# Kernel optimization log

Measured on AMD Instinct MI355X. Metric: run time of the kernel, lower is better.

The kernel has to match this reference:

```python
import jax, jax.numpy as jnp
import numpy as np


def setup_inputs() -> dict:
    key = jax.random.key(0)
    k1, k2, k3, k4 = jax.random.split(key, 4)
    B, L, T = 8, 2048, 1024
    Dh, Dg, Dp = 1024, 768, 256
    H = jax.random.normal(k1, (B, L, Dh), dtype=jnp.float32)
    G = jax.random.normal(k2, (B, T, Dg), dtype=jnp.float32)
    # nn.Linear(d_g, d_proj, bias=False).weight -> [d_proj, d_g]
    Wq = jax.random.normal(k3, (Dp, Dg), dtype=jnp.float32) * (Dg ** -0.5)
    Wk = jax.random.normal(k4, (Dp, Dh), dtype=jnp.float32) * (Dh ** -0.5)
    return {"H": H, "G": G, "Wq": Wq, "Wk": Wk}


def reference(H, G, Wq, Wk):
    # GO-token queries attend over protein residues; values are the raw H.
    # The torch module computes this with streaming chunks + online LSE,
    # which is mathematically identical to a single stable softmax attention.
    d_proj = Wq.shape[0]
    scale = d_proj ** -0.5
    Q = jnp.einsum('btg,pg->btp', G, Wq)          # [B,T,Dp]
    K = jnp.einsum('blh,ph->blp', H, Wk)          # [B,L,Dp]
    logits = jnp.einsum('btp,blp->btl', Q, K) * scale  # [B,T,L] fp32
    alpha = jax.nn.softmax(logits, axis=-1)
    # denominator clamp matches torch's s.clamp_min(1e-20) (no-op for unmasked)
    Z = jnp.einsum('btl,blh->bth', alpha, H)      # [B,T,Dh]
    return Z
```

## Files before the change

kernel.cpp:

```cpp
#include <hip/hip_runtime.h>
#include <hip/hip_bf16.h>
#include <type_traits>


typedef float    f32x4  __attribute__((ext_vector_type(4)));
typedef __bf16   bf16x8 __attribute__((ext_vector_type(8)));
typedef unsigned short u16x8 __attribute__((ext_vector_type(8)));

__device__ __forceinline__ unsigned short f2bf(float f) {
    union { __bf16 b; unsigned short u; } c;
    c.b = (__bf16)f;
    return c.u;
}
__device__ __forceinline__ float bf2f(unsigned short u) {
    union { unsigned u; float f; } x; x.u = ((unsigned)u) << 16;
    return x.f;
}
__device__ __forceinline__ void gload_lds16(const unsigned short* g, unsigned short* l) {
    __builtin_amdgcn_global_load_lds(
        (const __attribute__((address_space(1))) void*)g,
        (__attribute__((address_space(3))) void*)l, 16, 0, 0);
}

__global__ __launch_bounds__(256) void kn_castw(const float* __restrict__ Wq,
                                                const float* __restrict__ Wk,
                                                unsigned short* __restrict__ Wqbf,
                                                unsigned short* __restrict__ Wkbf,
                                                float* __restrict__ rowsum,
                                                int nq8, int nk8, int nrs4) {
    int tid = threadIdx.x;
    if (blockIdx.x == 0) {
        f32x4 z = {};
        for (int j = tid; j < nrs4; j += 256)
            *(f32x4*)(rowsum + (size_t)j * 4) = z;
    }
    int i = blockIdx.x * 256 + tid;
    const float* src;
    unsigned short* dst;
    int idx;
    if (i < nq8) { idx = i; src = Wq; dst = Wqbf; }
    else { idx = i - nq8; if (idx >= nk8) return; src = Wk; dst = Wkbf; }
    f32x4 a = *(const f32x4*)(src + (size_t)idx * 8);
    f32x4 b = *(const f32x4*)(src + (size_t)idx * 8 + 4);
    u16x8 o;
#pragma unroll
    for (int j = 0; j < 4; ++j) { o[j] = f2bf(a[j]); o[4 + j] = f2bf(b[j]); }
    *(u16x8*)(dst + (size_t)idx * 8) = o;
}

__global__ __launch_bounds__(256) void kn_transp(const float* __restrict__ H,
                                                 unsigned short* __restrict__ HT,
                                                 unsigned short* __restrict__ Hbf,
                                                 int L, int D) {
    __shared__ float tile[64][65];
    int b = blockIdx.z;
    const float* src = H + (size_t)b * L * D;
    unsigned short* dstT = HT + (size_t)b * L * D;
    unsigned short* dstN = Hbf + (size_t)b * L * D;
    int l0 = blockIdx.y * 64, d0 = blockIdx.x * 64;
    int rh = threadIdx.x >> 3;
    int c8 = (threadIdx.x & 7) * 8;

#pragma unroll
    for (int i = 0; i < 2; ++i) {
        int r = rh + i * 32;
        const float* p = &src[(size_t)(l0 + r) * D + d0 + c8];
        f32x4 v0 = *(const f32x4*)p;
        f32x4 v1 = *(const f32x4*)(p + 4);
        u16x8 o;
#pragma unroll
        for (int j = 0; j < 4; ++j) {
            o[j] = f2bf(v0[j]); o[4 + j] = f2bf(v1[j]);
            tile[r][c8 + j] = v0[j];
            tile[r][c8 + 4 + j] = v1[j];
        }
        *(u16x8*)&dstN[(size_t)(l0 + r) * D + d0 + c8] = o;
    }
    __syncthreads();
#pragma unroll
    for (int i = 0; i < 2; ++i) {
        int d = rh + i * 32;
        u16x8 o;
#pragma unroll
        for (int j = 0; j < 8; ++j) o[j] = f2bf(tile[c8 + j][d]);
        *(u16x8*)&dstT[(size_t)(d0 + d) * L + l0 + c8] = o;
    }
}

__device__ __forceinline__ void qproj_body(char* smem_raw,
                                           const float* __restrict__ A,
                                           const unsigned short* __restrict__ B,
                                           unsigned short* __restrict__ C,
                                           int N, int K, int t) {
    unsigned short* sA = (unsigned short*)smem_raw;
    unsigned short* sB = sA + 32 * 64;
    float* st = (float*)smem_raw;

    int tid = threadIdx.x;
    int by = t >> 1;
    int bx = t & 1;
    const float* Ab = A + (size_t)by * 32 * K;
    const unsigned short* Bb = B + (size_t)bx * 128 * K;

    int lane = tid & 63;
    int wid = tid >> 6;
    int lr = lane & 15;
    int lg = lane >> 4;
    int xoff = (lane & 7) << 3;

    f32x4 acc[2][2] = {};

    for (int k0 = 0; k0 < K; k0 += 64) {
#pragma unroll
        for (int c = 0; c < 4; ++c) {
            int ch = c * 256 + tid;
            int row = ch >> 3;
            int g8 = (ch & 7) ^ (row & 7);
            gload_lds16(Bb + (size_t)row * K + k0 + g8 * 8, sB + ch * 8);
        }
        {
            int ch = tid;
            int row = ch >> 3;
            const float* srcp = Ab + (size_t)row * K + k0 + (ch & 7) * 8;
            f32x4 v0 = *(const f32x4*)srcp;
            f32x4 v1 = *(const f32x4*)(srcp + 4);
            u16x8 o;
#pragma unroll
            for (int j = 0; j < 4; ++j) { o[j] = f2bf(v0[j]); o[4 + j] = f2bf(v1[j]); }
            int sl = (ch & 7) ^ (row & 7);
            *(u16x8*)&sA[row * 64 + sl * 8] = o;
        }
        __syncthreads();
#pragma unroll
        for (int kk = 0; kk < 2; ++kk) {
            int kb = (kk * 32 + lg * 8) ^ xoff;
            bf16x8 af[2], bfr[2];
#pragma unroll
            for (int m = 0; m < 2; ++m)
                af[m] = *(const bf16x8*)&sA[(m * 16 + lr) * 64 + kb];
#pragma unroll
            for (int n = 0; n < 2; ++n)
                bfr[n] = *(const bf16x8*)&sB[(wid * 32 + n * 16 + lr) * 64 + kb];
#pragma unroll
            for (int m = 0; m < 2; ++m)
#pragma unroll
                for (int n = 0; n < 2; ++n)
                    acc[m][n] = __builtin_amdgcn_mfma_f32_16x16x32_bf16(af[m], bfr[n], acc[m][n], 0, 0, 0);
        }
        __syncthreads();
    }

#pragma unroll
    for (int m = 0; m < 2; ++m) {
        int r0 = m * 16 + lg * 4;
#pragma unroll
        for (int n = 0; n < 2; ++n) {
            int c0 = wid * 32 + n * 16 + lr;
#pragma unroll
            for (int j = 0; j < 4; ++j)
                st[(r0 + j) * 132 + c0] = acc[m][n][j];
        }
    }
    __syncthreads();
    int r  = tid >> 3;
    int c0 = (tid & 7) * 16;
    size_t grow = (size_t)(by * 32 + r) * N + bx * 128 + c0;
#pragma unroll
    for (int g = 0; g < 2; ++g) {
        f32x4 a = *(const f32x4*)&st[r * 132 + c0 + g * 8];
        f32x4 b = *(const f32x4*)&st[r * 132 + c0 + g * 8 + 4];
        u16x8 o;
#pragma unroll
        for (int j = 0; j < 4; ++j) { o[j] = f2bf(a[j]); o[4 + j] = f2bf(b[j]); }
        *(u16x8*)&C[grow + g * 8] = o;
    }
}

__device__ __forceinline__ void kproj_body(char* smem_raw,
                                           const unsigned short* __restrict__ A,
                                           const unsigned short* __restrict__ B,
                                           unsigned short* __restrict__ C,
                                           int N, int K, int t) {
    unsigned short* sA = (unsigned short*)smem_raw;
    unsigned short* sB = sA + 64 * 64;
    float* st = (float*)smem_raw;

    int tid = threadIdx.x;
    int by = t >> 1;
    int bx = t & 1;
    const unsigned short* Ab = A + (size_t)by * 64 * K;
    const unsigned short* Bb = B + (size_t)bx * 128 * K;

    int lane = tid & 63;
    int wid = tid >> 6;
    int wr = wid >> 1, wc = wid & 1;
    int lr = lane & 15;
    int lg = lane >> 4;
    int xoff = (lane & 7) << 3;

    f32x4 acc[2][4] = {};

    for (int k0 = 0; k0 < K; k0 += 64) {
#pragma unroll
        for (int c = 0; c < 2; ++c) {
            int ch = c * 256 + tid;
            int row = ch >> 3;
            int g8 = (ch & 7) ^ (row & 7);
            gload_lds16(Ab + (size_t)row * K + k0 + g8 * 8, sA + ch * 8);
        }
#pragma unroll
        for (int c = 0; c < 4; ++c) {
            int ch = c * 256 + tid;
            int row = ch >> 3;
            int g8 = (ch & 7) ^ (row & 7);
            gload_lds16(Bb + (size_t)row * K + k0 + g8 * 8, sB + ch * 8);
        }
        __syncthreads();
#pragma unroll
        for (int kk = 0; kk < 2; ++kk) {
            int kb = (kk * 32 + lg * 8) ^ xoff;
            bf16x8 af[2], bfr[4];
#pragma unroll
            for (int m = 0; m < 2; ++m)
                af[m] = *(const bf16x8*)&sA[(wr * 32 + m * 16 + lr) * 64 + kb];
#pragma unroll
            for (int n = 0; n < 4; ++n)
                bfr[n] = *(const bf16x8*)&sB[(wc * 64 + n * 16 + lr) * 64 + kb];
#pragma unroll
            for (int m = 0; m < 2; ++m)
#pragma unroll
                for (int n = 0; n < 4; ++n)
                    acc[m][n] = __builtin_amdgcn_mfma_f32_16x16x32_bf16(af[m], bfr[n], acc[m][n], 0, 0, 0);
        }
        __syncthreads();
    }

#pragma unroll
    for (int m = 0; m < 2; ++m) {
        int r0 = wr * 32 + m * 16 + lg * 4;
#pragma unroll
        for (int n = 0; n < 4; ++n) {
            int c0 = wc * 64 + n * 16 + lr;
#pragma unroll
            for (int j = 0; j < 4; ++j)
                st[(r0 + j) * 132 + c0] = acc[m][n][j];
        }
    }
    __syncthreads();
    int r  = tid >> 2;
    int c0 = (tid & 3) * 32;
    size_t grow = (size_t)(by * 64 + r) * N + bx * 128 + c0;
#pragma unroll
    for (int g = 0; g < 4; ++g) {
        f32x4 a = *(const f32x4*)&st[r * 132 + c0 + g * 8];
        f32x4 b = *(const f32x4*)&st[r * 132 + c0 + g * 8 + 4];
        u16x8 o;
#pragma unroll
        for (int j = 0; j < 4; ++j) { o[j] = f2bf(a[j]); o[4 + j] = f2bf(b[j]); }
        *(u16x8*)&C[grow + g * 8] = o;
    }
}

__global__ __launch_bounds__(256) void kn_proj(const unsigned short* __restrict__ Hbf,
                                               const unsigned short* __restrict__ Wkbf,
                                               unsigned short* __restrict__ Kbf,
                                               const float* __restrict__ G,
                                               const unsigned short* __restrict__ Wqbf,
                                               unsigned short* __restrict__ Qbf,
                                               int Dp, int Dh, int Dg) {
    __shared__ __align__(16) char smem_raw[64 * 132 * 4];
    int wg = blockIdx.x;
    if (wg < 512) kproj_body(smem_raw, Hbf, Wkbf, Kbf, Dp, Dh, wg);
    else          qproj_body(smem_raw, G, Wqbf, Qbf, Dp, Dg, wg - 512);
}

__global__ __launch_bounds__(512) void kn_sgemm(const unsigned short* __restrict__ A,
                                                const unsigned short* __restrict__ B,
                                                unsigned short* __restrict__ C,
                                                float* __restrict__ rowsum,
                                                int N, int K, int Trows,
                                                long batchA, long batchB, long batchC,
                                                float scale, int gxs) {
    __shared__ __align__(16) char smem_raw[49152];
    unsigned short* base = (unsigned short*)smem_raw;
    float* st = (float*)smem_raw;

    int tid = threadIdx.x;
    int wg = blockIdx.x;
    int bz = wg & 7;
    int t = wg >> 3;
    int by = t >> gxs;
    int bx = t & ((1 << gxs) - 1);

    const unsigned short* Ab = A + (size_t)bz * batchA + (size_t)by * 256 * K;
    const unsigned short* Bb = B + (size_t)bz * batchB + (size_t)bx * 128 * K;
    unsigned short* Cb = C + (size_t)bz * batchC;
    float* rs = rowsum + (size_t)bz * Trows;

    int lane = tid & 63;
    int wid = tid >> 6;
    int wr = wid >> 1, wc = wid & 1;
    int lr = lane & 15;
    int lg = lane >> 4;
    int xoff = (lane & 7) << 3;

    f32x4 acc[4][4] = {};

    for (int k0 = 0; k0 < K; k0 += 64) {
#pragma unroll
        for (int c = 0; c < 6; ++c) {
            int ch = c * 512 + tid;
            if (ch < 2048) {
                int row = ch >> 3;
                int g8 = (ch & 7) ^ (row & 7);
                gload_lds16(Ab + (size_t)row * K + k0 + g8 * 8, base + ch * 8);
            } else {
                int bc = ch - 2048;
                int row = bc >> 3;
                int g8 = (bc & 7) ^ (row & 7);
                gload_lds16(Bb + (size_t)row * K + k0 + g8 * 8, base + 16384 + bc * 8);
            }
        }
        __syncthreads();
#pragma unroll
        for (int kk = 0; kk < 2; ++kk) {
            int kb = (kk * 32 + lg * 8) ^ xoff;
            bf16x8 af[4], bfr[4];
#pragma unroll
            for (int m = 0; m < 4; ++m)
                af[m] = *(const bf16x8*)&base[(wr * 64 + m * 16 + lr) * 64 + kb];
#pragma unroll
            for (int n = 0; n < 4; ++n)
                bfr[n] = *(const bf16x8*)&base[16384 + (wc * 64 + n * 16 + lr) * 64 + kb];
#pragma unroll
            for (int m = 0; m < 4; ++m)
#pragma unroll
                for (int n = 0; n < 4; ++n)
                    acc[m][n] = __builtin_amdgcn_mfma_f32_16x16x32_bf16(af[m], bfr[n], acc[m][n], 0, 0, 0);
        }
        __syncthreads();
    }

#pragma unroll
    for (int q = 0; q < 4; ++q) {
        if (wr == q) {
#pragma unroll
            for (int m = 0; m < 4; ++m) {
                int rl = m * 16 + lg * 4;
#pragma unroll
                for (int n = 0; n < 4; ++n) {
                    int col = wc * 64 + n * 16 + lr;
#pragma unroll
                    for (int j = 0; j < 4; ++j)
                        st[(rl + j) * 132 + col] = acc[m][n][j] * scale;
                }
            }
        }
        __syncthreads();
        int r = tid >> 3;
        int c0 = (tid & 7) * 16;
        int grow_r = by * 256 + q * 64 + r;
        size_t grow = (size_t)grow_r * N + bx * 128 + c0;
        float psum = 0.f;
#pragma unroll
        for (int g = 0; g < 2; ++g) {
            f32x4 a = *(const f32x4*)&st[r * 132 + c0 + g * 8];
            f32x4 b = *(const f32x4*)&st[r * 132 + c0 + g * 8 + 4];
            u16x8 o;
#pragma unroll
            for (int j = 0; j < 4; ++j) {
                o[j]     = f2bf(__expf(a[j]));
                o[4 + j] = f2bf(__expf(b[j]));
                psum += bf2f(o[j]) + bf2f(o[4 + j]);
            }
            *(u16x8*)&Cb[grow + g * 8] = o;
        }
        psum += __shfl_xor(psum, 1);
        psum += __shfl_xor(psum, 2);
        psum += __shfl_xor(psum, 4);
        if ((tid & 7) == 0)
            atomicAdd(&rs[grow_r], psum);
        __syncthreads();
    }
}

__global__ __launch_bounds__(512) void kn_pv(const unsigned short* __restrict__ A,
                                             const unsigned short* __restrict__ B,
                                             float* __restrict__ C,
                                             const float* __restrict__ rowsum,
                                             int N, int K, int Trows,
                                             long batchA, long batchB, long batchC,
                                             int gxs) {
    __shared__ __align__(16) char smem_raw[3 * 49152];
    unsigned short* base = (unsigned short*)smem_raw;
    float* st = (float*)smem_raw;

    int tid = threadIdx.x;
    int wg = blockIdx.x;
    int bz = wg & 7;
    int t = wg >> 3;
    int by = t >> gxs;
    int bx = t & ((1 << gxs) - 1);

    const unsigned short* Ab = A + (size_t)bz * batchA + (size_t)by * 256 * K;
    const unsigned short* Bb = B + (size_t)bz * batchB + (size_t)bx * 128 * K;
    float* Cb = C + (size_t)bz * batchC;
    const float* rs = rowsum + (size_t)bz * Trows;

    int lane = tid & 63;
    int wid = tid >> 6;
    int wr = wid >> 1, wc = wid & 1;
    int lr = lane & 15;
    int lg = lane >> 4;
    int xoff = (lane & 7) << 3;

    f32x4 acc[4][4] = {};
    bf16x8 fA0[4], fB0[4], fA1[4], fB1[4];

    auto STAGE_HALF = [&](int buf, int k0, int half) {
        unsigned short* dA = base + buf * 24576;
        unsigned short* dB = dA + 16384;
#pragma unroll
        for (int c = 0; c < 3; ++c) {
            int ch = half * 1536 + c * 512 + tid;
            if (ch < 2048) {
                int row = ch >> 3;
                int g8 = (ch & 7) ^ (row & 7);
                gload_lds16(Ab + (size_t)row * K + k0 + g8 * 8, dA + ch * 8);
            } else {
                int bc = ch - 2048;
                int row = bc >> 3;
                int g8 = (bc & 7) ^ (row & 7);
                gload_lds16(Bb + (size_t)row * K + k0 + g8 * 8, dB + bc * 8);
            }
        }
    };
    auto LDFRAG = [&](int buf, int kk, bf16x8* fa, bf16x8* fb) {
        unsigned short* pA = base + buf * 24576;
        unsigned short* pB = pA + 16384;
        int kb = (kk * 32 + lg * 8) ^ xoff;
#pragma unroll
        for (int m = 0; m < 4; ++m)
            fa[m] = *(const bf16x8*)&pA[(wr * 64 + m * 16 + lr) * 64 + kb];
#pragma unroll
        for (int n = 0; n < 4; ++n)
            fb[n] = *(const bf16x8*)&pB[(wc * 64 + n * 16 + lr) * 64 + kb];
    };

    int nt = K / 64;
    STAGE_HALF(0, 0, 0);   STAGE_HALF(0, 0, 1);
    STAGE_HALF(1, 64, 0);  STAGE_HALF(1, 64, 1);
    asm volatile("s_waitcnt vmcnt(6)" ::: "memory");
    __builtin_amdgcn_s_barrier();
    LDFRAG(0, 0, fA0, fB0);

    int cur = 0;
    for (int tt = 0; tt < nt; ++tt) {
        int nb  = (cur >= 1) ? cur - 1 : 2;
        int nxt = (cur == 2) ? 0 : cur + 1;
        if (tt + 2 < nt) STAGE_HALF(nb, (tt + 2) * 64, 0);
        LDFRAG(cur, 1, fA1, fB1);
        __builtin_amdgcn_sched_barrier(0);
        __builtin_amdgcn_s_setprio(1);
#pragma unroll
        for (int m = 0; m < 4; ++m)
#pragma unroll
            for (int n = 0; n < 4; ++n)
                acc[m][n] = __builtin_amdgcn_mfma_f32_16x16x32_bf16(fA0[m], fB0[n], acc[m][n], 0, 0, 0);
        __builtin_amdgcn_s_setprio(0);
        __builtin_amdgcn_sched_barrier(0);
        if (tt + 2 < nt) STAGE_HALF(nb, (tt + 2) * 64, 1);
        __builtin_amdgcn_sched_barrier(0);
        __builtin_amdgcn_s_setprio(1);
#pragma unroll
        for (int m = 0; m < 4; ++m)
#pragma unroll
            for (int n = 0; n < 4; ++n)
                acc[m][n] = __builtin_amdgcn_mfma_f32_16x16x32_bf16(fA1[m], fB1[n], acc[m][n], 0, 0, 0);
        __builtin_amdgcn_s_setprio(0);
        __builtin_amdgcn_sched_barrier(0);
        if (tt + 1 < nt) {
            if (tt + 2 < nt) asm volatile("s_waitcnt vmcnt(6)" ::: "memory");
            else             asm volatile("s_waitcnt vmcnt(0)" ::: "memory");
            LDFRAG(nxt, 0, fA0, fB0);
            __builtin_amdgcn_sched_barrier(0);
            __builtin_amdgcn_s_barrier();
        }
        cur = nxt;
    }
    __syncthreads();

#pragma unroll
    for (int q = 0; q < 4; ++q) {
        if (wr == q) {
#pragma unroll
            for (int m = 0; m < 4; ++m) {
                int rl = m * 16 + lg * 4;
#pragma unroll
                for (int n = 0; n < 4; ++n) {
                    int col = wc * 64 + n * 16 + lr;
#pragma unroll
                    for (int j = 0; j < 4; ++j)
                        st[(rl + j) * 132 + col] = acc[m][n][j];
                }
            }
        }
        __syncthreads();
        int r = tid >> 3;
        int c0 = (tid & 7) * 16;
        float inv = 1.0f / rs[by * 256 + q * 64 + r];
        size_t grow = (size_t)(by * 256 + q * 64 + r) * N + bx * 128 + c0;
#pragma unroll
        for (int g = 0; g < 4; ++g) {
            f32x4 v = *(const f32x4*)&st[r * 132 + c0 + g * 4];
#pragma unroll
            for (int j = 0; j < 4; ++j) v[j] *= inv;
            *(f32x4*)&Cb[grow + g * 4] = v;
        }
        __syncthreads();
    }
}

extern "C" void kernel_launch(void* const* d_in, const int* in_sizes, int n_in,
                              void* d_out, int out_size, void* d_ws, size_t ws_size,
                              hipStream_t stream) {
    constexpr int B = 8, L = 2048, T = 1024, Dh = 1024, Dg = 768, Dp = 256;
    const float* H  = (const float*)d_in[0];
    const float* G  = (const float*)d_in[1];
    const float* Wq = (const float*)d_in[2];
    const float* Wk = (const float*)d_in[3];
    float* Z = (float*)d_out;

    unsigned short* Qbf  = (unsigned short*)d_ws;
    unsigned short* Kbf  = Qbf + (size_t)B * T * Dp;
    unsigned short* HT   = Kbf + (size_t)B * L * Dp;
    unsigned short* S    = HT  + (size_t)B * Dh * L;
    unsigned short* Hbf  = S   + (size_t)B * T * L;
    unsigned short* Wqbf = Hbf + (size_t)B * L * Dh;
    unsigned short* Wkbf = Wqbf + (size_t)Dp * Dg;
    float* rowsum = (float*)(Wkbf + (size_t)Dp * Dh);

    int nq8 = Dp * Dg / 8, nk8 = Dp * Dh / 8;
    kn_castw<<<(nq8 + nk8 + 255) / 256, 256, 0, stream>>>
        (Wq, Wk, Wqbf, Wkbf, rowsum, nq8, nk8, B * T / 4);

    kn_transp<<<dim3(Dh / 64, L / 64, B), dim3(256), 0, stream>>>(H, HT, Hbf, L, Dh);

    kn_proj<<<1024, 256, 0, stream>>>(Hbf, Wkbf, Kbf, G, Wqbf, Qbf, Dp, Dh, Dg);

    kn_sgemm<<<(T / 256) * (L / 128) * B, 512, 0, stream>>>
        (Qbf, Kbf, S, rowsum, L, Dp, T, (long)T * Dp, (long)L * Dp, (long)T * L, 0.0625f, 4);

    kn_pv<<<(T / 256) * (Dh / 128) * B, 512, 0, stream>>>
        (S, HT, Z, rowsum, Dh, L, T, (long)T * L, (long)Dh * L, (long)T * Dh, 3);
}
```

Measured before the change: 124.2 us.

## Fold weight cast into transpose kernel and simplify PV GEMM to double buffering

Removes the separate weight-cast/rowsum-zero kernel launch by folding that work into the H transpose kernel, using flattened block ids. Replaces the PV GEMM's hand-scheduled triple-buffered pipeline (half-stage loads, register-prefetched fragments, setprio and sched barriers) with a plain double-buffered loop that issues the next stage and syncs once per iteration. This saves a launch and cuts LDS from 144KB to 96KB, which may allow more occupancy. The cost is weaker load/compute overlap and more full barriers in the main GEMM.

After: 119.3 us (median of 2 runs). -3.9%, faster.

```diff
diff --git a/kernel.cpp b/kernel.cpp
--- a/kernel.cpp
+++ b/kernel.cpp
@@ -22,36 +22,15 @@
         (__attribute__((address_space(3))) void*)l, 16, 0, 0);
 }
 
-__global__ __launch_bounds__(256) void kn_castw(const float* __restrict__ Wq,
-                                                const float* __restrict__ Wk,
-                                                unsigned short* __restrict__ Wqbf,
-                                                unsigned short* __restrict__ Wkbf,
-                                                float* __restrict__ rowsum,
-                                                int nq8, int nk8, int nrs4) {
-    int tid = threadIdx.x;
-    if (blockIdx.x == 0) {
-        f32x4 z = {};
-        for (int j = tid; j < nrs4; j += 256)
-            *(f32x4*)(rowsum + (size_t)j * 4) = z;
-    }
-    int i = blockIdx.x * 256 + tid;
-    const float* src;
-    unsigned short* dst;
-    int idx;
-    if (i < nq8) { idx = i; src = Wq; dst = Wqbf; }
-    else { idx = i - nq8; if (idx >= nk8) return; src = Wk; dst = Wkbf; }
-    f32x4 a = *(const f32x4*)(src + (size_t)idx * 8);
-    f32x4 b = *(const f32x4*)(src + (size_t)idx * 8 + 4);
-    u16x8 o;
-#pragma unroll
-    for (int j = 0; j < 4; ++j) { o[j] = f2bf(a[j]); o[4 + j] = f2bf(b[j]); }
-    *(u16x8*)(dst + (size_t)idx * 8) = o;
-}
-
 __global__ __launch_bounds__(256) void kn_transp(const float* __restrict__ H,
                                                  unsigned short* __restrict__ HT,
                                                  unsigned short* __restrict__ Hbf,
-                                                 int L, int D) {
+                                                 const float* __restrict__ Wq,
+                                                 const float* __restrict__ Wk,
+                                                 unsigned short* __restrict__ Wqbf,
+                                                 unsigned short* __restrict__ Wkbf,
+                                                 float* __restrict__ rowsum,
+                                                 int L, int D, int nq8, int nk8, int nrs4) {
     __shared__ float tile[64][65];
     int b = blockIdx.z;
     const float* src = H + (size_t)b * L * D;
@@ -60,6 +39,29 @@
     int l0 = blockIdx.y * 64, d0 = blockIdx.x * 64;
     int rh = threadIdx.x >> 3;
     int c8 = (threadIdx.x & 7) * 8;
+
+    int fid = blockIdx.x + gridDim.x * (blockIdx.y + gridDim.y * blockIdx.z);
+    if (fid == 0) {
+        f32x4 z = {};
+        for (int j = threadIdx.x; j < nrs4; j += 256)
+            *(f32x4*)(rowsum + (size_t)j * 4) = z;
+    }
+    {
+        int i = fid * 256 + threadIdx.x;
+        if (i < nq8 + nk8) {
+            const float* s;
+            unsigned short* dp;
+            int idx;
+            if (i < nq8) { idx = i; s = Wq; dp = Wqbf; }
+            else         { idx = i - nq8; s = Wk; dp = Wkbf; }
+            f32x4 a = *(const f32x4*)(s + (size_t)idx * 8);
+            f32x4 bb = *(const f32x4*)(s + (size_t)idx * 8 + 4);
+            u16x8 o;
+#pragma unroll
+            for (int j = 0; j < 4; ++j) { o[j] = f2bf(a[j]); o[4 + j] = f2bf(bb[j]); }
+            *(u16x8*)(dp + (size_t)idx * 8) = o;
+        }
+    }
 
 #pragma unroll
     for (int i = 0; i < 2; ++i) {
@@ -391,7 +393,7 @@
                                              int N, int K, int Trows,
                                              long batchA, long batchB, long batchC,
                                              int gxs) {
-    __shared__ __align__(16) char smem_raw[3 * 49152];
+    __shared__ __align__(16) char smem_raw[2 * 49152];
     unsigned short* base = (unsigned short*)smem_raw;
     float* st = (float*)smem_raw;
 
@@ -415,14 +417,13 @@
     int xoff = (lane & 7) << 3;
 
     f32x4 acc[4][4] = {};
-    bf16x8 fA0[4], fB0[4], fA1[4], fB1[4];
-
-    auto STAGE_HALF = [&](int buf, int k0, int half) {
+
+    auto STAGE = [&](int buf, int k0) {
         unsigned short* dA = base + buf * 24576;
         unsigned short* dB = dA + 16384;
 #pragma unroll
-        for (int c = 0; c < 3; ++c) {
-            int ch = half * 1536 + c * 512 + tid;
+        for (int c = 0; c < 6; ++c) {
+            int ch = c * 512 + tid;
             if (ch < 2048) {
                 int row = ch >> 3;
                 int g8 = (ch & 7) ^ (row & 7);
@@ -435,60 +436,37 @@
             }
         }
     };
-    auto LDFRAG = [&](int buf, int kk, bf16x8* fa, bf16x8* fb) {
+    auto COMPUTE = [&](int buf) {
         unsigned short* pA = base + buf * 24576;
         unsigned short* pB = pA + 16384;
-        int kb = (kk * 32 + lg * 8) ^ xoff;
-#pragma unroll
-        for (int m = 0; m < 4; ++m)
-            fa[m] = *(const bf16x8*)&pA[(wr * 64 + m * 16 + lr) * 64 + kb];
-#pragma unroll
-        for (int n = 0; n < 4; ++n)
-            fb[n] = *(const bf16x8*)&pB[(wc * 64 + n * 16 + lr) * 64 + kb];
+#pragma unroll
+        for (int kk = 0; kk < 2; ++kk) {
+            int kb = (kk * 32 + lg * 8) ^ xoff;
+            bf16x8 af[4], bfr[4];
+#pragma unroll
+            for (int m = 0; m < 4; ++m)
+                af[m] = *(const bf16x8*)&pA[(wr * 64 + m * 16 + lr) * 64 + kb];
+#pragma unroll
+            for (int n = 0; n < 4; ++n)
+                bfr[n] = *(const bf16x8*)&pB[(wc * 64 + n * 16 + lr) * 64 + kb];
+#pragma unroll
+            for (int m = 0; m < 4; ++m)
+#pragma unroll
+                for (int n = 0; n < 4; ++n)
+                    acc[m][n] = __builtin_amdgcn_mfma_f32_16x16x32_bf16(af[m], bfr[n], acc[m][n], 0, 0, 0);
+        }
     };
 
     int nt = K / 64;
-    STAGE_HALF(0, 0, 0);   STAGE_HALF(0, 0, 1);
-    STAGE_HALF(1, 64, 0);  STAGE_HALF(1, 64, 1);
-    asm volatile("s_waitcnt vmcnt(6)" ::: "memory");
-    __builtin_amdgcn_s_barrier();
-    LDFRAG(0, 0, fA0, fB0);
-
+    STAGE(0, 0);
+    __syncthreads();
     int cur = 0;
     for (int tt = 0; tt < nt; ++tt) {
-        int nb  = (cur >= 1) ? cur - 1 : 2;
-        int nxt = (cur == 2) ? 0 : cur + 1;
-        if (tt + 2 < nt) STAGE_HALF(nb, (tt + 2) * 64, 0);
-        LDFRAG(cur, 1, fA1, fB1);
-        __builtin_amdgcn_sched_barrier(0);
-        __builtin_amdgcn_s_setprio(1);
-#pragma unroll
-        for (int m = 0; m < 4; ++m)
-#pragma unroll
-            for (int n = 0; n < 4; ++n)
-                acc[m][n] = __builtin_amdgcn_mfma_f32_16x16x32_bf16(fA0[m], fB0[n], acc[m][n], 0, 0, 0);
-        __builtin_amdgcn_s_setprio(0);
-        __builtin_amdgcn_sched_barrier(0);
-        if (tt + 2 < nt) STAGE_HALF(nb, (tt + 2) * 64, 1);
-        __builtin_amdgcn_sched_barrier(0);
-        __builtin_amdgcn_s_setprio(1);
-#pragma unroll
-        for (int m = 0; m < 4; ++m)
-#pragma unroll
-            for (int n = 0; n < 4; ++n)
-                acc[m][n] = __builtin_amdgcn_mfma_f32_16x16x32_bf16(fA1[m], fB1[n], acc[m][n], 0, 0, 0);
-        __builtin_amdgcn_s_setprio(0);
-        __builtin_amdgcn_sched_barrier(0);
-        if (tt + 1 < nt) {
-            if (tt + 2 < nt) asm volatile("s_waitcnt vmcnt(6)" ::: "memory");
-            else             asm volatile("s_waitcnt vmcnt(0)" ::: "memory");
-            LDFRAG(nxt, 0, fA0, fB0);
-            __builtin_amdgcn_sched_barrier(0);
-            __builtin_amdgcn_s_barrier();
-        }
-        cur = nxt;
-    }
-    __syncthreads();
+        if (tt + 1 < nt) STAGE(cur ^ 1, (tt + 1) * 64);
+        COMPUTE(cur);
+        __syncthreads();
+        cur ^= 1;
+    }
 
 #pragma unroll
     for (int q = 0; q < 4; ++q) {
@@ -541,10 +519,9 @@
     float* rowsum = (float*)(Wkbf + (size_t)Dp * Dh);
 
     int nq8 = Dp * Dg / 8, nk8 = Dp * Dh / 8;
-    kn_castw<<<(nq8 + nk8 + 255) / 256, 256, 0, stream>>>
-        (Wq, Wk, Wqbf, Wkbf, rowsum, nq8, nk8, B * T / 4);
-
-    kn_transp<<<dim3(Dh / 64, L / 64, B), dim3(256), 0, stream>>>(H, HT, Hbf, L, Dh);
+
+    kn_transp<<<dim3(Dh / 64, L / 64, B), dim3(256), 0, stream>>>
+        (H, HT, Hbf, Wq, Wk, Wqbf, Wkbf, rowsum, L, Dh, nq8, nk8, B * T / 4);
 
     kn_proj<<<1024, 256, 0, stream>>>(Hbf, Wkbf, Kbf, G, Wqbf, Qbf, Dp, Dh, Dg);
 
```
